# Optimization experiments

Hardware: AMD Instinct MI355X
Metric: run time of the kernel (lower is better)

Reference implementation:

```python
import jax, jax.numpy as jnp
import numpy as np

N_NODES = 100000
N_EDGES = 1600000
IN_DIM, HID, OUT_DIM = 8, 64, 32
LN_EPS = 1e-5


def _layer_norm(x, g, b):
    m = jnp.mean(x, axis=-1, keepdims=True)
    v = jnp.var(x, axis=-1, keepdims=True)
    return g * (x - m) / jnp.sqrt(v + LN_EPS) + b


def _gat(h, W, a, src, dst, n_nodes):
    # Wh: [N, H]
    Wh = h @ W
    # per-edge score: dot(Wh[src], Wh[dst]) * sum(a)  (leaky relu, slope 0.2)
    s = jnp.sum(Wh[src] * Wh[dst], axis=-1)  # [E]
    e = jax.nn.leaky_relu(s * jnp.sum(a), negative_slope=0.2)
    att = jax.nn.softmax(e)  # NOTE: global softmax over ALL edges, as in source
    msg = att[:, None] * Wh[src]  # [E, H]
    h_prime = jax.ops.segment_sum(msg, dst, num_segments=n_nodes)
    return jax.nn.elu(h_prime)


def _stack(x, src, dst, params):
    out = x
    for (W, a, g, b) in params:
        out = _layer_norm(_gat(out, W, a, src, dst, N_NODES), g, b)
    return out


def setup_inputs() -> dict:
    key = jax.random.key(0)
    ks = jax.random.split(key, 24)
    d = {}
    d['x'] = jax.random.normal(ks[0], (N_NODES, IN_DIM), dtype=jnp.float32)
    d['edge_index'] = jax.random.randint(ks[1], (2, N_EDGES), 0, N_NODES, dtype=jnp.int32)
    d['edge_type'] = jax.random.randint(ks[2], (N_EDGES,), 0, 2, dtype=jnp.int32)
    d['temporal_edge_index'] = jax.random.randint(ks[3], (2, N_EDGES), 0, N_NODES, dtype=jnp.int32)

    def xavier(k, shape):
        fan_in, fan_out = shape[0], shape[1]
        lim = float(np.sqrt(6.0 / (fan_in + fan_out)))
        return jax.random.uniform(k, shape, jnp.float32, -lim, lim)

    i = 4
    for pfx in ('s', 't'):
        for li, ind in enumerate((IN_DIM, HID)):
            d[f'{pfx}W{li}'] = xavier(ks[i], (ind, HID)); i += 1
            d[f'{pfx}a{li}'] = xavier(ks[i], (2 * HID, 1)); i += 1
            d[f'{pfx}g{li}'] = jnp.ones((HID,), jnp.float32)
            d[f'{pfx}b{li}'] = jnp.zeros((HID,), jnp.float32)
    d['cW1'] = xavier(ks[i], (HID, OUT_DIM)); i += 1
    d['cb1'] = jnp.zeros((OUT_DIM,), jnp.float32)
    d['cW2'] = xavier(ks[i], (OUT_DIM, 1)); i += 1
    d['cb2'] = jnp.zeros((1,), jnp.float32)
    return d


def reference(x, edge_index, edge_type, temporal_edge_index,
              sW0, sa0, sg0, sb0, sW1, sa1, sg1, sb1,
              tW0, ta0, tg0, tb0, tW1, ta1, tg1, tb1,
              cW1, cb1, cW2, cb2):
    sp = _stack(x, edge_index[0], edge_index[1],
                [(sW0, sa0, sg0, sb0), (sW1, sa1, sg1, sb1)])
    tp = _stack(x, temporal_edge_index[0], temporal_edge_index[1],
                [(tW0, ta0, tg0, tb0), (tW1, ta1, tg1, tb1)])
    h = sp + tp
    h = jax.nn.relu(h @ cW1 + cb1)
    return jax.nn.sigmoid(h @ cW2 + cb2)  # [N, 1]
```

## Files before the change

### kernel.cpp

```cpp
#include <hip/hip_runtime.h>
#include <math.h>

#define NN 100000
#define NE 1600000
#define HID 64
#define NBE 2048
#define NBG 2048
#define NBF 2048
#define EPB 2048
#define NBLK 782
#define NBUCK 98
#define MATN (2 * NBUCK * NBLK)
#define ESHIFT 30.0f

__global__ void prep4(const float* __restrict__ a0, const float* __restrict__ a1,
                      const float* __restrict__ a2, const float* __restrict__ a3,
                      float* __restrict__ sum_a) {
    int w = threadIdx.x >> 6, lane = threadIdx.x & 63;
    const float* a = (w == 0) ? a0 : (w == 1) ? a1 : (w == 2) ? a2 : a3;
    float v = a[lane] + a[lane + 64];
    #pragma unroll
    for (int o = 32; o >= 1; o >>= 1) v += __shfl_xor(v, o);
    if (lane == 0) sum_a[w] = v;
}

__global__ void bucket_hist(const int* __restrict__ eiS, const int* __restrict__ eiT,
                            int* __restrict__ cnt) {
    __shared__ int hist[NBUCK];
    int t = threadIdx.x;
    int side = blockIdx.x >= NBLK;
    int blk = blockIdx.x - side * NBLK;
    const int* dst = (side ? eiT : eiS) + NE;
    if (t < NBUCK) hist[t] = 0;
    __syncthreads();
    int base = blk * EPB;
    #pragma unroll
    for (int k = 0; k < EPB / 256; k++) {
        int e = base + k * 256 + t;
        if (e < NE) atomicAdd(&hist[dst[e] >> 10], 1);
    }
    __syncthreads();
    if (t < NBUCK) cnt[side * (NBUCK * NBLK) + t * NBLK + blk] = hist[t];
}

__global__ void scanA(const int* __restrict__ deg, int* __restrict__ rowtmp,
                      int* __restrict__ bsum, int n) {
    __shared__ int sh[256];
    int t = threadIdx.x;
    int base = blockIdx.x * 1024 + t * 4;
    int a0 = (base + 0 < n) ? deg[base + 0] : 0;
    int a1 = (base + 1 < n) ? deg[base + 1] : 0;
    int a2 = (base + 2 < n) ? deg[base + 2] : 0;
    int a3 = (base + 3 < n) ? deg[base + 3] : 0;
    int s = a0 + a1 + a2 + a3;
    sh[t] = s;
    __syncthreads();
    for (int off = 1; off < 256; off <<= 1) {
        int x = (t >= off) ? sh[t - off] : 0;
        __syncthreads();
        sh[t] += x;
        __syncthreads();
    }
    int excl = sh[t] - s;
    if (t == 255) bsum[blockIdx.x] = sh[255];
    if (base + 0 < n) rowtmp[base + 0] = excl;
    if (base + 1 < n) rowtmp[base + 1] = excl + a0;
    if (base + 2 < n) rowtmp[base + 2] = excl + a0 + a1;
    if (base + 3 < n) rowtmp[base + 3] = excl + a0 + a1 + a2;
}

__global__ void scanB(int* __restrict__ bsum, int nb) {
    __shared__ int sh[256];
    int t = threadIdx.x;
    int v = (t < nb) ? bsum[t] : 0;
    sh[t] = v;
    __syncthreads();
    for (int off = 1; off < 256; off <<= 1) {
        int x = (t >= off) ? sh[t - off] : 0;
        __syncthreads();
        sh[t] += x;
        __syncthreads();
    }
    if (t < nb) bsum[t] = sh[t] - v;
}

__global__ void scanC(const int* __restrict__ rowtmp, const int* __restrict__ bsum,
                      int* __restrict__ outp, int n, int total) {
    int i = blockIdx.x * 256 + threadIdx.x;
    if (i < n) outp[i] = rowtmp[i] + bsum[i >> 10];
    if (i == n) outp[n] = total;
}

__global__ void bucket_scatter(const int* __restrict__ eiS, const int* __restrict__ eiT,
                               const int* __restrict__ off, int2* __restrict__ part) {
    __shared__ int cur[NBUCK];
    int t = threadIdx.x;
    int side = blockIdx.x >= NBLK;
    int blk = blockIdx.x - side * NBLK;
    const int* ei = side ? eiT : eiS;
    if (t < NBUCK) cur[t] = off[side * (NBUCK * NBLK) + t * NBLK + blk];
    __syncthreads();
    int base = blk * EPB;
    #pragma unroll
    for (int k = 0; k < EPB / 256; k++) {
        int e = base + k * 256 + t;
        if (e < NE) {
            int s = ei[e], d = ei[NE + e];
            int p = atomicAdd(&cur[d >> 10], 1);
            part[p] = make_int2(s, d);
        }
    }
}

__global__ void bucket_csr(const int2* __restrict__ part, const int* __restrict__ off,
                           int* __restrict__ rowptrS, int* __restrict__ rowptrT,
                           int* __restrict__ csrsS, int* __restrict__ csrsT) {
    __shared__ int hist[1024];
    __shared__ int sh[1024];
    int t = threadIdx.x;
    int g = blockIdx.x;
    int side = g >= NBUCK;
    int bin = g - side * NBUCK;
    int start = off[g * NBLK];
    int end = off[(g + 1) * NBLK];
    hist[t] = 0;
    __syncthreads();
    for (int i = start + t; i < end; i += 1024)
        atomicAdd(&hist[part[i].y & 1023], 1);
    __syncthreads();
    int own = hist[t];
    sh[t] = own;
    __syncthreads();
    for (int o = 1; o < 1024; o <<= 1) {
        int x = (t >= o) ? sh[t - o] : 0;
        __syncthreads();
        sh[t] += x;
        __syncthreads();
    }
    int excl = sh[t] - own;
    int node = bin * 1024 + t;
    int* rowptr = side ? rowptrT : rowptrS;
    if (node < NN) rowptr[node] = (start - side * NE) + excl;
    if (t == 0 && bin == NBUCK - 1) rowptr[NN] = NE;
    __syncthreads();
    hist[t] = start + excl;
    __syncthreads();
    int* csr = side ? csrsT : csrsS;
    int sub = side * NE;
    for (int i = start + t; i < end; i += 1024) {
        int2 e = part[i];
        int p = atomicAdd(&hist[e.y & 1023], 1);
        csr[p - sub] = e.x;
    }
}

__global__ void gemm2_k8(const float* __restrict__ x, const float* __restrict__ WS,
                         const float* __restrict__ WT, float* __restrict__ WhS,
                         float* __restrict__ WhT, int n) {
    const int nbh = (NN + 63) / 64;
    int side = blockIdx.x >= nbh;
    int blk = blockIdx.x - side * nbh;
    const float* W = side ? WT : WS;
    float* Wh = side ? WhT : WhS;
    __shared__ float Wl[8][HID];
    int t = threadIdx.x;
    for (int i = t; i < 8 * HID / 4; i += 256)
        ((float4*)Wl)[i] = ((const float4*)W)[i];
    __syncthreads();
    int node = blk * 64 + (t >> 2);
    int c0 = (t & 3) * 16;
    if (node >= n) return;
    float acc[16];
    #pragma unroll
    for (int j = 0; j < 16; j++) acc[j] = 0.f;
    const float* hr = x + (size_t)node * 8;
    #pragma unroll
    for (int k4 = 0; k4 < 2; k4++) {
        float4 hv = *(const float4*)(hr + k4 * 4);
        #pragma unroll
        for (int j = 0; j < 16; j++)
            acc[j] += hv.x * Wl[k4*4+0][c0+j] + hv.y * Wl[k4*4+1][c0+j]
                    + hv.z * Wl[k4*4+2][c0+j] + hv.w * Wl[k4*4+3][c0+j];
    }
    float* o = Wh + (size_t)node * HID + c0;
    #pragma unroll
    for (int j = 0; j < 16; j += 4)
        *(float4*)(o + j) = make_float4(acc[j], acc[j+1], acc[j+2], acc[j+3]);
}

__global__ void edge_agg2(const float* __restrict__ WhS, const float* __restrict__ WhT,
                          const int* __restrict__ rowptrS, const int* __restrict__ rowptrT,
                          const int* __restrict__ csrsS, const int* __restrict__ csrsT,
                          const float* __restrict__ sum_a, int aiS, int aiT,
                          float* __restrict__ accS, float* __restrict__ accT,
                          float* __restrict__ bsumz, int n) {
    int side = blockIdx.x >= NBE;
    int blk = blockIdx.x - side * NBE;
    const float* Wh = side ? WhT : WhS;
    const int* rowptr = side ? rowptrT : rowptrS;
    const int* csrs = side ? csrsT : csrsS;
    float* acc = side ? accT : accS;
    float sa = sum_a[side ? aiT : aiS];
    int t = threadIdx.x;
    int w = t >> 6, lane = t & 63;
    int g = lane >> 3, l8 = lane & 7;
    float Zw = 0.f;
    for (int node = blk * 4 + w; node < n; node += NBE * 4) {
        const float* qp = Wh + (size_t)node * HID + l8 * 8;
        float4 q0 = *(const float4*)qp, q1 = *(const float4*)(qp + 4);
        int beg = rowptr[node], end = rowptr[node + 1];
        float z = 0.f;
        float4 a0 = make_float4(0,0,0,0), a1 = make_float4(0,0,0,0);
        for (int i = beg; i < end; i += 8) {
            int idx = i + g;
            bool act = idx < end;
            int s = csrs[act ? idx : beg];
            const float* vp = Wh + (size_t)s * HID + l8 * 8;
            float4 v0 = *(const float4*)vp, v1 = *(const float4*)(vp + 4);
            float x = q0.x*v0.x + q0.y*v0.y + q0.z*v0.z + q0.w*v0.w
                    + q1.x*v1.x + q1.y*v1.y + q1.z*v1.z + q1.w*v1.w;
            x += __shfl_xor(x, 1); x += __shfl_xor(x, 2); x += __shfl_xor(x, 4);
            float e = x * sa;
            e = e > 0.f ? e : 0.2f * e;
            float wg = act ? __expf(e - ESHIFT) : 0.f;
            z += wg;
            a0.x += wg*v0.x; a0.y += wg*v0.y; a0.z += wg*v0.z; a0.w += wg*v0.w;
            a1.x += wg*v1.x; a1.y += wg*v1.y; a1.z += wg*v1.z; a1.w += wg*v1.w;
        }
        #pragma unroll
        for (int o = 8; o <= 32; o <<= 1) {
            z    += __shfl_xor(z, o);
            a0.x += __shfl_xor(a0.x, o); a0.y += __shfl_xor(a0.y, o);
            a0.z += __shfl_xor(a0.z, o); a0.w += __shfl_xor(a0.w, o);
            a1.x += __shfl_xor(a1.x, o); a1.y += __shfl_xor(a1.y, o);
            a1.z += __shfl_xor(a1.z, o); a1.w += __shfl_xor(a1.w, o);
        }
        if (g == 0) {
            float* ap = acc + (size_t)node * HID + l8 * 8;
            *(float4*)ap = a0; *(float4*)(ap + 4) = a1;
        }
        Zw += z;
    }
    __shared__ float shz[4];
    if (lane == 0) shz[w] = Zw;
    __syncthreads();
    if (t == 0) bsumz[blockIdx.x] = (shz[0] + shz[1]) + (shz[2] + shz[3]);
}

__device__ __forceinline__ float combine_invZ(const float* __restrict__ bsumz,
                                              int base, float* shred) {
    int t = threadIdx.x;
    float lz = 0.f;
    for (int i = t; i < NBE; i += 256) lz += bsumz[base + i];
    #pragma unroll
    for (int o = 32; o >= 1; o >>= 1) lz += __shfl_xor(lz, o);
    if ((t & 63) == 0) shred[t >> 6] = lz;
    __syncthreads();
    float Zt = (shred[0] + shred[1]) + (shred[2] + shred[3]);
    __syncthreads();
    return 1.f / Zt;
}

__global__ void normgemm2(const float* __restrict__ accS, const float* __restrict__ accT,
                          const float* __restrict__ bsumz,
                          const float* __restrict__ gS, const float* __restrict__ bS,
                          const float* __restrict__ gT, const float* __restrict__ bT,
                          const float* __restrict__ W1S, const float* __restrict__ W1T,
                          float* __restrict__ WhS, float* __restrict__ WhT, int n) {
    int side = blockIdx.x >= NBG;
    int blk = blockIdx.x - side * NBG;
    const float* acc = side ? accT : accS;
    const float* g = side ? gT : gS;
    const float* b = side ? bT : bS;
    const float* W1 = side ? W1T : W1S;
    float* Wh = side ? WhT : WhS;
    __shared__ float shred[4];
    float invZ = combine_invZ(bsumz, side * NBE, shred);
    __shared__ float Wl[64 * 64];
    int t = threadIdx.x;
    for (int i = t; i < 1024; i += 256)
        ((float4*)Wl)[i] = ((const float4*)W1)[i];
    __syncthreads();
    __shared__ float hrow[4][64];
    int w = t >> 6, lane = t & 63;
    float gl = g[lane], bl = b[lane];
    for (int node = blk * 4 + w; node < n; node += NBG * 4) {
        float v = acc[(size_t)node * HID + lane] * invZ;
        v = v > 0.f ? v : expm1f(v);
        float s = v, s2 = v * v;
        #pragma unroll
        for (int o = 32; o >= 1; o >>= 1) {
            s += __shfl_xor(s, o);
            s2 += __shfl_xor(s2, o);
        }
        float mean = s * (1.f / 64.f);
        float var = s2 * (1.f / 64.f) - mean * mean;
        float hn = gl * (v - mean) * rsqrtf(var + 1e-5f) + bl;
        hrow[w][lane] = hn;
        float o2 = 0.f;
        #pragma unroll
        for (int k = 0; k < 64; k++) o2 += hrow[w][k] * Wl[k * 64 + lane];
        Wh[(size_t)node * HID + lane] = o2;
    }
}

__global__ void normfinal(const float* __restrict__ accS, const float* __restrict__ accT,
                          const float* __restrict__ bsumz,
                          const float* __restrict__ gS, const float* __restrict__ bS,
                          const float* __restrict__ gT, const float* __restrict__ bT,
                          const float* __restrict__ cW1, const float* __restrict__ cb1,
                          const float* __restrict__ cW2, const float* __restrict__ cb2,
                          float* __restrict__ out, int n) {
    __shared__ float shred[4];
    float invZS = combine_invZ(bsumz, 0, shred);
    float invZT = combine_invZ(bsumz, NBE, shred);
    __shared__ float W1l[64 * 32];
    __shared__ float W2l[32], B1l[32];
    int t = threadIdx.x;
    for (int i = t; i < 512; i += 256)
        ((float4*)W1l)[i] = ((const float4*)cW1)[i];
    if (t < 32) { W2l[t] = cW2[t]; B1l[t] = cb1[t]; }
    __syncthreads();
    float c2 = cb2[0];
    __shared__ float hrow[4][64];
    int w = t >> 6, lane = t & 63;
    int j = lane & 31;
    float glS = gS[lane], blS = bS[lane], glT = gT[lane], blT = bT[lane];
    for (int node = blockIdx.x * 4 + w; node < n; node += NBF * 4) {
        float vS = accS[(size_t)node * HID + lane] * invZS;
        vS = vS > 0.f ? vS : expm1f(vS);
        float sA = vS, sB = vS * vS;
        #pragma unroll
        for (int o = 32; o >= 1; o >>= 1) { sA += __shfl_xor(sA, o); sB += __shfl_xor(sB, o); }
        float meanS = sA * (1.f / 64.f);
        float varS = sB * (1.f / 64.f) - meanS * meanS;
        float hS = glS * (vS - meanS) * rsqrtf(varS + 1e-5f) + blS;
        float vT = accT[(size_t)node * HID + lane] * invZT;
        vT = vT > 0.f ? vT : expm1f(vT);
        sA = vT; sB = vT * vT;
        #pragma unroll
        for (int o = 32; o >= 1; o >>= 1) { sA += __shfl_xor(sA, o); sB += __shfl_xor(sB, o); }
        float meanT = sA * (1.f / 64.f);
        float varT = sB * (1.f / 64.f) - meanT * meanT;
        float hT = glT * (vT - meanT) * rsqrtf(varT + 1e-5f) + blT;
        hrow[w][lane] = hS + hT;
        float a = B1l[j];
        #pragma unroll
        for (int k = 0; k < 64; k++) a += hrow[w][k] * W1l[k * 32 + j];
        a = fmaxf(a, 0.f);
        float p = a * W2l[j];
        #pragma unroll
        for (int o = 16; o >= 1; o >>= 1) p += __shfl_xor(p, o, 32);
        if (lane == 0) out[node] = 1.f / (1.f + expf(-(p + c2)));
    }
}

extern "C" void kernel_launch(void* const* d_in, const int* in_sizes, int n_in,
                              void* d_out, int out_size, void* d_ws, size_t ws_size,
                              hipStream_t stream) {
    const float* x   = (const float*)d_in[0];
    const int*   ei  = (const int*)d_in[1];
    const int*   tei = (const int*)d_in[3];
    const float* sW0 = (const float*)d_in[4],  *sa0 = (const float*)d_in[5];
    const float* sg0 = (const float*)d_in[6],  *sb0 = (const float*)d_in[7];
    const float* sW1 = (const float*)d_in[8],  *sa1 = (const float*)d_in[9];
    const float* sg1 = (const float*)d_in[10], *sb1 = (const float*)d_in[11];
    const float* tW0 = (const float*)d_in[12], *ta0 = (const float*)d_in[13];
    const float* tg0 = (const float*)d_in[14], *tb0 = (const float*)d_in[15];
    const float* tW1 = (const float*)d_in[16], *ta1 = (const float*)d_in[17];
    const float* tg1 = (const float*)d_in[18], *tb1 = (const float*)d_in[19];
    const float* cW1 = (const float*)d_in[20], *cb1 = (const float*)d_in[21];
    const float* cW2 = (const float*)d_in[22], *cb2 = (const float*)d_in[23];
    float* out = (float*)d_out;

    float* ws = (float*)d_ws;
    size_t o = 0;
    float* hS  = ws + o; o += (size_t)NN * HID;
    float* hT  = ws + o; o += (size_t)NN * HID;
    float* WhS = ws + o; o += (size_t)NN * HID;
    float* WhT = ws + o; o += (size_t)NN * HID;
    float* bsumz = ws + o; o += 2 * NBE;
    float* sum_a = ws + o; o += 4;
    int* ip = (int*)(ws + o);
    int* rowptrS = ip; ip += NN + 1;
    int* rowptrT = ip; ip += NN + 1;
    int* csrsS   = ip; ip += NE;
    int* csrsT   = ip; ip += NE;

    int2* part   = (int2*)WhS;
    int*  cnt    = (int*)WhT;
    int*  offm   = cnt + (MATN + 1);
    int*  rowtmp = offm + (MATN + 1);
    int*  bsum   = rowtmp + MATN;

    const int NSB = (MATN + 1023) / 1024;

    bucket_hist<<<2 * NBLK, 256, 0, stream>>>(ei, tei, cnt);
    scanA<<<NSB, 256, 0, stream>>>(cnt, rowtmp, bsum, MATN);
    scanB<<<1, 256, 0, stream>>>(bsum, NSB);
    scanC<<<(MATN + 256) / 256, 256, 0, stream>>>(rowtmp, bsum, offm, MATN, 2 * NE);
    bucket_scatter<<<2 * NBLK, 256, 0, stream>>>(ei, tei, offm, part);
    bucket_csr<<<2 * NBUCK, 1024, 0, stream>>>(part, offm, rowptrS, rowptrT, csrsS, csrsT);

    prep4<<<1, 256, 0, stream>>>(sa0, sa1, ta0, ta1, sum_a);

    const int nbh = (NN + 63) / 64;

    gemm2_k8<<<2 * nbh, 256, 0, stream>>>(x, sW0, tW0, WhS, WhT, NN);
    edge_agg2<<<2 * NBE, 256, 0, stream>>>(WhS, WhT, rowptrS, rowptrT, csrsS, csrsT,
                                           sum_a, 0, 2, hS, hT, bsumz, NN);
    normgemm2<<<2 * NBG, 256, 0, stream>>>(hS, hT, bsumz,
                                           sg0, sb0, tg0, tb0, sW1, tW1, WhS, WhT, NN);
    edge_agg2<<<2 * NBE, 256, 0, stream>>>(WhS, WhT, rowptrS, rowptrT, csrsS, csrsT,
                                           sum_a, 1, 3, hS, hT, bsumz, NN);
    normfinal<<<NBF, 256, 0, stream>>>(hS, hT, bsumz,
                                       sg1, sb1, tg1, tb1, cW1, cb1, cW2, cb2, out, NN);
}
```

Measured before the change: 465.8 us.

## Pack edge partition entries, vectorize index loads, add nontemporal hints, fold prep kernel

Packs each bucketed edge into one 32-bit word (source index plus local destination), halving partition traffic. Edge index reads in the histogram and scatter kernels become 128-bit vector loads. The attention-vector summation is merged into the single-block scan kernel to drop one launch. Nontemporal load/store hints are added across the CSR build, GEMM and aggregation kernels, which may hurt if the data would otherwise be reused from cache.

Result: slower. 562.9 us (+20.9%).

```diff
diff --git a/kernel.cpp b/kernel.cpp
--- a/kernel.cpp
+++ b/kernel.cpp
@@ -13,16 +13,8 @@
 #define MATN (2 * NBUCK * NBLK)
 #define ESHIFT 30.0f
 
-__global__ void prep4(const float* __restrict__ a0, const float* __restrict__ a1,
-                      const float* __restrict__ a2, const float* __restrict__ a3,
-                      float* __restrict__ sum_a) {
-    int w = threadIdx.x >> 6, lane = threadIdx.x & 63;
-    const float* a = (w == 0) ? a0 : (w == 1) ? a1 : (w == 2) ? a2 : a3;
-    float v = a[lane] + a[lane + 64];
-    #pragma unroll
-    for (int o = 32; o >= 1; o >>= 1) v += __shfl_xor(v, o);
-    if (lane == 0) sum_a[w] = v;
-}
+typedef float f32x4 __attribute__((ext_vector_type(4)));
+typedef int   i32x4 __attribute__((ext_vector_type(4)));
 
 __global__ void bucket_hist(const int* __restrict__ eiS, const int* __restrict__ eiT,
                             int* __restrict__ cnt) {
@@ -30,14 +22,20 @@
     int t = threadIdx.x;
     int side = blockIdx.x >= NBLK;
     int blk = blockIdx.x - side * NBLK;
-    const int* dst = (side ? eiT : eiS) + NE;
+    const i32x4* dst4 = (const i32x4*)((side ? eiT : eiS) + NE);
     if (t < NBUCK) hist[t] = 0;
     __syncthreads();
-    int base = blk * EPB;
-    #pragma unroll
-    for (int k = 0; k < EPB / 256; k++) {
-        int e = base + k * 256 + t;
-        if (e < NE) atomicAdd(&hist[dst[e] >> 10], 1);
+    int base4 = blk * (EPB / 4);
+    #pragma unroll
+    for (int k = 0; k < EPB / 1024; k++) {
+        int i4 = base4 + k * 256 + t;
+        if (i4 < NE / 4) {
+            i32x4 d = __builtin_nontemporal_load(&dst4[i4]);
+            atomicAdd(&hist[d.x >> 10], 1);
+            atomicAdd(&hist[d.y >> 10], 1);
+            atomicAdd(&hist[d.z >> 10], 1);
+            atomicAdd(&hist[d.w >> 10], 1);
+        }
     }
     __syncthreads();
     if (t < NBUCK) cnt[side * (NBUCK * NBLK) + t * NBLK + blk] = hist[t];
@@ -69,7 +67,10 @@
     if (base + 3 < n) rowtmp[base + 3] = excl + a0 + a1 + a2;
 }
 
-__global__ void scanB(int* __restrict__ bsum, int nb) {
+__global__ void scanB(int* __restrict__ bsum, int nb,
+                      const float* __restrict__ a0, const float* __restrict__ a1,
+                      const float* __restrict__ a2, const float* __restrict__ a3,
+                      float* __restrict__ sum_a) {
     __shared__ int sh[256];
     int t = threadIdx.x;
     int v = (t < nb) ? bsum[t] : 0;
@@ -82,6 +83,12 @@
         __syncthreads();
     }
     if (t < nb) bsum[t] = sh[t] - v;
+    int w = t >> 6, lane = t & 63;
+    const float* a = (w == 0) ? a0 : (w == 1) ? a1 : (w == 2) ? a2 : a3;
+    float av = a[lane] + a[lane + 64];
+    #pragma unroll
+    for (int o = 32; o >= 1; o >>= 1) av += __shfl_xor(av, o);
+    if (lane == 0) sum_a[w] = av;
 }
 
 __global__ void scanC(const int* __restrict__ rowtmp, const int* __restrict__ bsum,
@@ -92,7 +99,7 @@
 }
 
 __global__ void bucket_scatter(const int* __restrict__ eiS, const int* __restrict__ eiT,
-                               const int* __restrict__ off, int2* __restrict__ part) {
+                               const int* __restrict__ off, unsigned* __restrict__ part) {
     __shared__ int cur[NBUCK];
     int t = threadIdx.x;
     int side = blockIdx.x >= NBLK;
@@ -100,19 +107,27 @@
     const int* ei = side ? eiT : eiS;
     if (t < NBUCK) cur[t] = off[side * (NBUCK * NBLK) + t * NBLK + blk];
     __syncthreads();
-    int base = blk * EPB;
-    #pragma unroll
-    for (int k = 0; k < EPB / 256; k++) {
-        int e = base + k * 256 + t;
-        if (e < NE) {
-            int s = ei[e], d = ei[NE + e];
-            int p = atomicAdd(&cur[d >> 10], 1);
-            part[p] = make_int2(s, d);
-        }
-    }
-}
-
-__global__ void bucket_csr(const int2* __restrict__ part, const int* __restrict__ off,
+    int base4 = blk * (EPB / 4);
+    #pragma unroll
+    for (int k = 0; k < EPB / 1024; k++) {
+        int i4 = base4 + k * 256 + t;
+        if (i4 < NE / 4) {
+            i32x4 s = __builtin_nontemporal_load(&((const i32x4*)ei)[i4]);
+            i32x4 d = __builtin_nontemporal_load(&((const i32x4*)(ei + NE))[i4]);
+            int p;
+            p = atomicAdd(&cur[d.x >> 10], 1);
+            __builtin_nontemporal_store((unsigned)s.x | ((unsigned)(d.x & 1023) << 17), &part[p]);
+            p = atomicAdd(&cur[d.y >> 10], 1);
+            __builtin_nontemporal_store((unsigned)s.y | ((unsigned)(d.y & 1023) << 17), &part[p]);
+            p = atomicAdd(&cur[d.z >> 10], 1);
+            __builtin_nontemporal_store((unsigned)s.z | ((unsigned)(d.z & 1023) << 17), &part[p]);
+            p = atomicAdd(&cur[d.w >> 10], 1);
+            __builtin_nontemporal_store((unsigned)s.w | ((unsigned)(d.w & 1023) << 17), &part[p]);
+        }
+    }
+}
+
+__global__ void bucket_csr(const unsigned* __restrict__ part, const int* __restrict__ off,
                            int* __restrict__ rowptrS, int* __restrict__ rowptrT,
                            int* __restrict__ csrsS, int* __restrict__ csrsT) {
     __shared__ int hist[1024];
@@ -125,8 +140,10 @@
     int end = off[(g + 1) * NBLK];
     hist[t] = 0;
     __syncthreads();
-    for (int i = start + t; i < end; i += 1024)
-        atomicAdd(&hist[part[i].y & 1023], 1);
+    for (int i = start + t; i < end; i += 1024) {
+        unsigned u = __builtin_nontemporal_load(&part[i]);
+        atomicAdd(&hist[u >> 17], 1);
+    }
     __syncthreads();
     int own = hist[t];
     sh[t] = own;
@@ -148,9 +165,9 @@
     int* csr = side ? csrsT : csrsS;
     int sub = side * NE;
     for (int i = start + t; i < end; i += 1024) {
-        int2 e = part[i];
-        int p = atomicAdd(&hist[e.y & 1023], 1);
-        csr[p - sub] = e.x;
+        unsigned u = __builtin_nontemporal_load(&part[i]);
+        int p = atomicAdd(&hist[u >> 17], 1);
+        csr[p - sub] = (int)(u & 0x1FFFFu);
     }
 }
 
@@ -176,7 +193,7 @@
     const float* hr = x + (size_t)node * 8;
     #pragma unroll
     for (int k4 = 0; k4 < 2; k4++) {
-        float4 hv = *(const float4*)(hr + k4 * 4);
+        f32x4 hv = __builtin_nontemporal_load((const f32x4*)(hr + k4 * 4));
         #pragma unroll
         for (int j = 0; j < 16; j++)
             acc[j] += hv.x * Wl[k4*4+0][c0+j] + hv.y * Wl[k4*4+1][c0+j]
@@ -214,7 +231,7 @@
         for (int i = beg; i < end; i += 8) {
             int idx = i + g;
             bool act = idx < end;
-            int s = csrs[act ? idx : beg];
+            int s = __builtin_nontemporal_load(&csrs[act ? idx : beg]);
             const float* vp = Wh + (size_t)s * HID + l8 * 8;
             float4 v0 = *(const float4*)vp, v1 = *(const float4*)(vp + 4);
             float x = q0.x*v0.x + q0.y*v0.y + q0.z*v0.z + q0.w*v0.w
@@ -237,7 +254,10 @@
         }
         if (g == 0) {
             float* ap = acc + (size_t)node * HID + l8 * 8;
-            *(float4*)ap = a0; *(float4*)(ap + 4) = a1;
+            f32x4 w0 = { a0.x, a0.y, a0.z, a0.w };
+            f32x4 w1 = { a1.x, a1.y, a1.z, a1.w };
+            __builtin_nontemporal_store(w0, (f32x4*)ap);
+            __builtin_nontemporal_store(w1, (f32x4*)(ap + 4));
         }
         Zw += z;
     }
@@ -285,7 +305,7 @@
     int w = t >> 6, lane = t & 63;
     float gl = g[lane], bl = b[lane];
     for (int node = blk * 4 + w; node < n; node += NBG * 4) {
-        float v = acc[(size_t)node * HID + lane] * invZ;
+        float v = __builtin_nontemporal_load(&acc[(size_t)node * HID + lane]) * invZ;
         v = v > 0.f ? v : expm1f(v);
         float s = v, s2 = v * v;
         #pragma unroll
@@ -327,7 +347,7 @@
     int j = lane & 31;
     float glS = gS[lane], blS = bS[lane], glT = gT[lane], blT = bT[lane];
     for (int node = blockIdx.x * 4 + w; node < n; node += NBF * 4) {
-        float vS = accS[(size_t)node * HID + lane] * invZS;
+        float vS = __builtin_nontemporal_load(&accS[(size_t)node * HID + lane]) * invZS;
         vS = vS > 0.f ? vS : expm1f(vS);
         float sA = vS, sB = vS * vS;
         #pragma unroll
@@ -335,7 +355,7 @@
         float meanS = sA * (1.f / 64.f);
         float varS = sB * (1.f / 64.f) - meanS * meanS;
         float hS = glS * (vS - meanS) * rsqrtf(varS + 1e-5f) + blS;
-        float vT = accT[(size_t)node * HID + lane] * invZT;
+        float vT = __builtin_nontemporal_load(&accT[(size_t)node * HID + lane]) * invZT;
         vT = vT > 0.f ? vT : expm1f(vT);
         sA = vT; sB = vT * vT;
         #pragma unroll
@@ -387,7 +407,7 @@
     int* csrsS   = ip; ip += NE;
     int* csrsT   = ip; ip += NE;
 
-    int2* part   = (int2*)WhS;
+    unsigned* part = (unsigned*)WhS;
     int*  cnt    = (int*)WhT;
     int*  offm   = cnt + (MATN + 1);
     int*  rowtmp = offm + (MATN + 1);
@@ -397,12 +417,10 @@
 
     bucket_hist<<<2 * NBLK, 256, 0, stream>>>(ei, tei, cnt);
     scanA<<<NSB, 256, 0, stream>>>(cnt, rowtmp, bsum, MATN);
-    scanB<<<1, 256, 0, stream>>>(bsum, NSB);
+    scanB<<<1, 256, 0, stream>>>(bsum, NSB, sa0, sa1, ta0, ta1, sum_a);
     scanC<<<(MATN + 256) / 256, 256, 0, stream>>>(rowtmp, bsum, offm, MATN, 2 * NE);
     bucket_scatter<<<2 * NBLK, 256, 0, stream>>>(ei, tei, offm, part);
     bucket_csr<<<2 * NBUCK, 1024, 0, stream>>>(part, offm, rowptrS, rowptrT, csrsS, csrsT);
-
-    prep4<<<1, 256, 0, stream>>>(sa0, sa1, ta0, ta1, sum_a);
 
     const int nbh = (NN + 63) / 64;
 
```
